# Optimization experiments

Measured on AMD Instinct MI355X. Metric: run time of the kernel, lower is better.

Reference implementation:

```python
import jax, jax.numpy as jnp
import numpy as np
import math

D_IN = 1024
D_OUT = 1024
NUM_HEADS = 16
D_HEAD = D_IN // NUM_HEADS


def setup_inputs() -> dict:
    key = jax.random.key(0)
    k1, k2, k3 = jax.random.split(key, 3)
    x = jax.random.normal(k1, (4, 2048, D_IN), dtype=jnp.float32)
    W_qkv = jax.random.normal(k2, (D_IN, 3 * D_OUT), dtype=jnp.float32) * (1.0 / math.sqrt(D_IN))
    b_qkv = jax.random.normal(k3, (3 * D_OUT,), dtype=jnp.float32) * 0.01
    return {"x": x, "W_qkv": W_qkv, "b_qkv": b_qkv}


def reference(x, W_qkv, b_qkv):
    B, S, _ = x.shape
    H, Dh = NUM_HEADS, D_HEAD
    # QKV projection: [B, S, 3*d_out]
    qkv = jnp.einsum('bsd,de->bse', x, W_qkv) + b_qkv
    # reshape per original: (B, S, H, 3*Dh) -> (B, H, S, 3*Dh)
    qkv = qkv.reshape(B, S, H, 3 * Dh).transpose(0, 2, 1, 3)
    q, k, v = jnp.split(qkv, 3, axis=-1)  # each [B, H, S, Dh]
    scale = 1.0 / math.sqrt(Dh)
    scores = jnp.einsum('bhqd,bhkd->bhqk', q, k) * scale
    attn = jax.nn.softmax(scores, axis=-1)
    ctx = jnp.einsum('bhqk,bhkd->bhqd', attn, v)  # [B, H, S, Dh]
    # (B, H, S, Dh) -> (B, S, H*Dh)
    return ctx.transpose(0, 2, 1, 3).reshape(B, S, D_OUT)
```

## Files before the change

### kernel.cpp

```cpp
#include <hip/hip_runtime.h>
#include <stdint.h>
#include <math.h>

#define D_IN   1024
#define NQKV   3072
#define NHEADS 16
#define DH     64
#define BATCH  4
#define SEQ    2048
#define MTOT   (BATCH*SEQ)

typedef __bf16    bf16x8 __attribute__((ext_vector_type(8)));
typedef _Float16  f16x8  __attribute__((ext_vector_type(8)));
typedef float     f32x4  __attribute__((ext_vector_type(4)));

typedef __attribute__((address_space(3))) unsigned short       lds_us;
typedef __attribute__((address_space(1))) const unsigned short glb_us;

__device__ __forceinline__ unsigned short f2bf(float f) {
    union { float f; uint32_t u; } c; c.f = f;
    uint32_t u = c.u;
    uint32_t r = u + 0x7fffu + ((u >> 16) & 1u);
    return (unsigned short)(r >> 16);
}
__device__ __forceinline__ float bf2f(unsigned short b) {
    union { uint32_t u; float f; } c; c.u = ((uint32_t)b) << 16;
    return c.f;
}
__device__ __forceinline__ uint32_t pkh(float a, float b) {
    auto h = __builtin_amdgcn_cvt_pkrtz(a, b);
    uint32_t u;
    __builtin_memcpy(&u, &h, 4);
    return u;
}

__global__ void k_convert_x(const float* __restrict__ x, unsigned short* __restrict__ xb) {
    int i = blockIdx.x * 256 + threadIdx.x;
    float4 v = ((const float4*)x)[i];
    ushort4 o;
    o.x = f2bf(v.x); o.y = f2bf(v.y); o.z = f2bf(v.z); o.w = f2bf(v.w);
    ((ushort4*)xb)[i] = o;
}

__global__ void k_convert_wt(const float* __restrict__ W, unsigned short* __restrict__ Wt) {
    __shared__ float tile[32][33];
    int tx = threadIdx.x, ty = threadIdx.y;
    int n0 = blockIdx.x * 32, k0 = blockIdx.y * 32;
    #pragma unroll
    for (int i = 0; i < 4; ++i) {
        int k = k0 + ty + i*8;
        tile[ty + i*8][tx] = W[(size_t)k * NQKV + n0 + tx];
    }
    __syncthreads();
    #pragma unroll
    for (int i = 0; i < 4; ++i) {
        int n = n0 + ty + i*8;
        Wt[(size_t)n * D_IN + k0 + tx] = f2bf(tile[tx][ty + i*8]);
    }
}

__global__ __launch_bounds__(256) void k_gemm_qkv(
    const unsigned short* __restrict__ A,
    const unsigned short* __restrict__ Bt,
    const float* __restrict__ bias,
    unsigned short* __restrict__ C)
{
    __shared__ __align__(16) unsigned short As[128*32];
    __shared__ __align__(16) unsigned short Bs[128*32];
    const int t = threadIdx.x;
    const int wave = t >> 6, lane = t & 63, quad = lane >> 4, l15 = lane & 15;
    const int wm = wave >> 1, wn = wave & 1;
    const int m0 = blockIdx.y * 128, n0 = blockIdx.x * 128;
    const int crow = lane >> 2;
    const int ccol = (lane & 3) << 3;

    f32x4 acc[4][4] = {};
    lds_us* As3 = (lds_us*)As;
    lds_us* Bs3 = (lds_us*)Bs;

    for (int k0 = 0; k0 < D_IN; k0 += 32) {
        #pragma unroll
        for (int j = 0; j < 2; ++j) {
            int chunk = wave*2 + j;
            const unsigned short* ga = A  + (size_t)(m0 + chunk*16 + crow)*D_IN + k0 + ccol;
            const unsigned short* gb = Bt + (size_t)(n0 + chunk*16 + crow)*D_IN + k0 + ccol;
            __builtin_amdgcn_global_load_lds((glb_us*)ga, As3 + chunk*512, 16, 0, 0);
            __builtin_amdgcn_global_load_lds((glb_us*)gb, Bs3 + chunk*512, 16, 0, 0);
        }
        __syncthreads();
        bf16x8 a[4], b[4];
        #pragma unroll
        for (int tm = 0; tm < 4; ++tm)
            a[tm] = *(const bf16x8*)(&As[(wm*64 + tm*16 + l15)*32 + quad*8]);
        #pragma unroll
        for (int tn = 0; tn < 4; ++tn)
            b[tn] = *(const bf16x8*)(&Bs[(wn*64 + tn*16 + l15)*32 + quad*8]);
        #pragma unroll
        for (int tm = 0; tm < 4; ++tm)
            #pragma unroll
            for (int tn = 0; tn < 4; ++tn)
                acc[tm][tn] = __builtin_amdgcn_mfma_f32_16x16x32_bf16(a[tm], b[tn], acc[tm][tn], 0, 0, 0);
        __syncthreads();
    }
    const float qs = 0.125f * 1.44269504089f;
    #pragma unroll
    for (int tn = 0; tn < 4; ++tn) {
        int col = n0 + wn*64 + tn*16 + l15;
        float bv = bias[col];
        float s = ((col % 192) < 64) ? qs : 1.0f;
        #pragma unroll
        for (int tm = 0; tm < 4; ++tm) {
            #pragma unroll
            for (int r = 0; r < 4; ++r) {
                int row = m0 + wm*64 + tm*16 + quad*4 + r;
                C[(size_t)row*NQKV + col] = f2bf((acc[tm][tn][r] + bv) * s);
            }
        }
    }
}

#define TP 66
__global__ __launch_bounds__(256) void k_transpose_v(
    const unsigned short* __restrict__ qkv,
    unsigned short* __restrict__ vtg)
{
    __shared__ unsigned short T[64*TP];
    const int t = threadIdx.x;
    const int bh = blockIdx.y, b = bh >> 4, h = bh & 15;
    const int s0 = blockIdx.x * 64;
    const unsigned short* src = qkv + (size_t)(b*SEQ + s0)*NQKV + h*(3*DH) + 2*DH;
    #pragma unroll
    for (int i = 0; i < 2; ++i) {
        int idx = t + i*256;
        int s = idx >> 3, c = (idx & 7) << 3;
        uint4 v = *(const uint4*)(src + (size_t)s*NQKV + c);
        unsigned short* dst = &T[s*TP + c];
        const unsigned short* pv = (const unsigned short*)&v;
        #pragma unroll
        for (int j = 0; j < 8; ++j) {
            _Float16 hv = (_Float16)bf2f(pv[j]);
            dst[j] = *(unsigned short*)&hv;
        }
    }
    __syncthreads();
    unsigned short* out = vtg + (size_t)bh * DH * SEQ + s0;
    #pragma unroll
    for (int i = 0; i < 16; ++i) {
        int idx = t + i*256;
        int d = idx >> 6, s = idx & 63;
        out[(size_t)d * SEQ + s] = T[s*TP + d];
    }
}

#define PPAD 40
#define OPAD 72
__global__ __launch_bounds__(256, 2) void k_attn(
    const unsigned short* __restrict__ qkv,
    const unsigned short* __restrict__ vtg,
    float* __restrict__ out)
{
    __shared__ __align__(16) unsigned short PO[4*64*OPAD];
    __shared__ float Lp[4*64];

    const int t = threadIdx.x;
    const int wave = t >> 6, lane = t & 63, quad = lane >> 4, l15 = lane & 15;
    const int bh = blockIdx.y, b = bh >> 4, h = bh & 15;
    const int m0 = blockIdx.x * 64;
    const unsigned short* base  = qkv + (size_t)(b*SEQ)*NQKV + h*(3*DH);
    const unsigned short* kbase = base + DH;
    const unsigned short* vbase = vtg + (size_t)bh * DH * SEQ;

    bf16x8 qb[4][2];
    #pragma unroll
    for (int tq = 0; tq < 4; ++tq) {
        const unsigned short* qrow = base + (size_t)(m0 + tq*16 + l15) * NQKV;
        qb[tq][0] = *(const bf16x8*)(qrow + quad*8);
        qb[tq][1] = *(const bf16x8*)(qrow + 32 + quad*8);
    }

    f32x4 o[4][4] = {};
    float lp[4] = {0.f, 0.f, 0.f, 0.f};
    unsigned short* pw = &PO[wave*64*PPAD];

    bf16x8 kf[2][2][2];
    f16x8  vf[2][4];
    {
        int key0 = wave*32;
        #pragma unroll
        for (int tk = 0; tk < 2; ++tk) {
            const unsigned short* kr = kbase + (size_t)(key0 + tk*16 + l15)*NQKV;
            kf[0][tk][0] = *(const bf16x8*)(kr + quad*8);
            kf[0][tk][1] = *(const bf16x8*)(kr + 32 + quad*8);
        }
        #pragma unroll
        for (int td = 0; td < 4; ++td)
            vf[0][td] = *(const f16x8*)(vbase + (size_t)(td*16 + l15)*SEQ + key0 + quad*8);
    }

    #pragma unroll 2
    for (int it = 0; it < 16; ++it) {
        const int cur = it & 1, nxt = cur ^ 1;
        if (it < 15) {
            int key0 = (it+1)*128 + wave*32;
            #pragma unroll
            for (int tk = 0; tk < 2; ++tk) {
                const unsigned short* kr = kbase + (size_t)(key0 + tk*16 + l15)*NQKV;
                kf[nxt][tk][0] = *(const bf16x8*)(kr + quad*8);
                kf[nxt][tk][1] = *(const bf16x8*)(kr + 32 + quad*8);
            }
            #pragma unroll
            for (int td = 0; td < 4; ++td)
                vf[nxt][td] = *(const f16x8*)(vbase + (size_t)(td*16 + l15)*SEQ + key0 + quad*8);
        }
        #pragma unroll
        for (int tk = 0; tk < 2; ++tk) {
            #pragma unroll
            for (int tq = 0; tq < 4; ++tq) {
                f32x4 a = {};
                a = __builtin_amdgcn_mfma_f32_16x16x32_bf16(kf[cur][tk][0], qb[tq][0], a, 0, 0, 0);
                a = __builtin_amdgcn_mfma_f32_16x16x32_bf16(kf[cur][tk][1], qb[tq][1], a, 0, 0, 0);
                float p0 = exp2f(a[0]), p1 = exp2f(a[1]);
                float p2 = exp2f(a[2]), p3 = exp2f(a[3]);
                lp[tq] += (p0 + p1) + (p2 + p3);
                uint2 u; u.x = pkh(p0, p1); u.y = pkh(p2, p3);
                *(uint2*)(&pw[(tq*16 + l15)*PPAD + tk*16 + quad*4]) = u;
            }
        }
        f16x8 pb[4];
        #pragma unroll
        for (int tq = 0; tq < 4; ++tq)
            pb[tq] = *(const f16x8*)(&pw[(tq*16 + l15)*PPAD + quad*8]);
        #pragma unroll
        for (int td = 0; td < 4; ++td)
            #pragma unroll
            for (int tq = 0; tq < 4; ++tq)
                o[td][tq] = __builtin_amdgcn_mfma_f32_16x16x32_f16(vf[cur][td], pb[tq], o[td][tq], 0, 0, 0);
    }

    #pragma unroll
    for (int tq = 0; tq < 4; ++tq) {
        float s = lp[tq];
        s += __shfl_xor(s, 16);
        s += __shfl_xor(s, 32);
        if (quad == 0) Lp[wave*64 + tq*16 + l15] = s;
    }
    __syncthreads();
    {
        unsigned short* ow = &PO[wave*64*OPAD];
        #pragma unroll
        for (int td = 0; td < 4; ++td)
            #pragma unroll
            for (int tq = 0; tq < 4; ++tq) {
                uint2 u; u.x = pkh(o[td][tq][0], o[td][tq][1]); u.y = pkh(o[td][tq][2], o[td][tq][3]);
                *(uint2*)(&ow[(tq*16 + l15)*OPAD + td*16 + quad*4]) = u;
            }
    }
    __syncthreads();
    float* outb = out + (size_t)(b*SEQ + m0) * (NHEADS*DH) + h*DH;
    #pragma unroll
    for (int i = 0; i < 16; ++i) {
        int idx = t + i*256;
        int q = idx >> 6, d = idx & 63;
        float lt = Lp[q] + Lp[64 + q] + Lp[128 + q] + Lp[192 + q];
        float s = 0.f;
        #pragma unroll
        for (int w2 = 0; w2 < 4; ++w2) {
            _Float16 hv = *(const _Float16*)&PO[(w2*64 + q)*OPAD + d];
            s += (float)hv;
        }
        outb[(size_t)q * (NHEADS*DH) + d] = s / lt;
    }
}

extern "C" void kernel_launch(void* const* d_in, const int* in_sizes, int n_in,
                              void* d_out, int out_size, void* d_ws, size_t ws_size,
                              hipStream_t stream) {
    const float* x    = (const float*)d_in[0];
    const float* W    = (const float*)d_in[1];
    const float* bias = (const float*)d_in[2];
    float* out = (float*)d_out;

    unsigned short* xb  = (unsigned short*)d_ws;
    unsigned short* Wt  = xb  + (size_t)MTOT * D_IN;
    unsigned short* qkv = Wt  + (size_t)NQKV * D_IN;
    unsigned short* vtg = xb;

    hipLaunchKernelGGL(k_convert_x,   dim3(MTOT*D_IN/4/256), dim3(256),    0, stream, x, xb);
    hipLaunchKernelGGL(k_convert_wt,  dim3(NQKV/32, D_IN/32), dim3(32, 8), 0, stream, W, Wt);
    hipLaunchKernelGGL(k_gemm_qkv,    dim3(NQKV/128, MTOT/128), dim3(256), 0, stream, xb, Wt, bias, qkv);
    hipLaunchKernelGGL(k_transpose_v, dim3(SEQ/64, BATCH*NHEADS), dim3(256), 0, stream, qkv, vtg);
    hipLaunchKernelGGL(k_attn,        dim3(SEQ/64, BATCH*NHEADS), dim3(256), 0, stream, qkv, vtg, out);
}
```

Before: 299.3 us.

## Single-buffer K/V fragments with staggered prefetch, raise occupancy, add MFMA priority

The attention loop drops its double-buffered K/V register fragments. Each K tile is now reloaded right after its QK MFMAs, and V is reloaded after the PV MFMAs, which cuts register pressure so launch bounds can request 3 blocks per CU. MFMA sections are wrapped in s_setprio so matrix work is favoured across waves. The grid is also transposed so blocks that share a head are spread across the first dimension, which changes L2 locality. The cost is less latency hiding per wave, since loads now land only one phase ahead, and more reliance on occupancy to cover it.

```diff
diff --git a/kernel.cpp b/kernel.cpp
--- a/kernel.cpp
+++ b/kernel.cpp
@@ -126,8 +126,8 @@
 {
     __shared__ unsigned short T[64*TP];
     const int t = threadIdx.x;
-    const int bh = blockIdx.y, b = bh >> 4, h = bh & 15;
-    const int s0 = blockIdx.x * 64;
+    const int bh = blockIdx.x, b = bh >> 4, h = bh & 15;
+    const int s0 = blockIdx.y * 64;
     const unsigned short* src = qkv + (size_t)(b*SEQ + s0)*NQKV + h*(3*DH) + 2*DH;
     #pragma unroll
     for (int i = 0; i < 2; ++i) {
@@ -154,7 +154,7 @@
 
 #define PPAD 40
 #define OPAD 72
-__global__ __launch_bounds__(256, 2) void k_attn(
+__global__ __launch_bounds__(256, 3) void k_attn(
     const unsigned short* __restrict__ qkv,
     const unsigned short* __restrict__ vtg,
     float* __restrict__ out)
@@ -164,8 +164,8 @@
 
     const int t = threadIdx.x;
     const int wave = t >> 6, lane = t & 63, quad = lane >> 4, l15 = lane & 15;
-    const int bh = blockIdx.y, b = bh >> 4, h = bh & 15;
-    const int m0 = blockIdx.x * 64;
+    const int bh = blockIdx.x, b = bh >> 4, h = bh & 15;
+    const int m0 = blockIdx.y * 64;
     const unsigned short* base  = qkv + (size_t)(b*SEQ)*NQKV + h*(3*DH);
     const unsigned short* kbase = base + DH;
     const unsigned short* vbase = vtg + (size_t)bh * DH * SEQ;
@@ -182,59 +182,59 @@
     float lp[4] = {0.f, 0.f, 0.f, 0.f};
     unsigned short* pw = &PO[wave*64*PPAD];
 
-    bf16x8 kf[2][2][2];
-    f16x8  vf[2][4];
+    bf16x8 kf[2][2];
+    f16x8  vf[4];
     {
         int key0 = wave*32;
         #pragma unroll
         for (int tk = 0; tk < 2; ++tk) {
             const unsigned short* kr = kbase + (size_t)(key0 + tk*16 + l15)*NQKV;
-            kf[0][tk][0] = *(const bf16x8*)(kr + quad*8);
-            kf[0][tk][1] = *(const bf16x8*)(kr + 32 + quad*8);
+            kf[tk][0] = *(const bf16x8*)(kr + quad*8);
+            kf[tk][1] = *(const bf16x8*)(kr + 32 + quad*8);
         }
         #pragma unroll
         for (int td = 0; td < 4; ++td)
-            vf[0][td] = *(const f16x8*)(vbase + (size_t)(td*16 + l15)*SEQ + key0 + quad*8);
-    }
-
-    #pragma unroll 2
+            vf[td] = *(const f16x8*)(vbase + (size_t)(td*16 + l15)*SEQ + key0 + quad*8);
+    }
+
     for (int it = 0; it < 16; ++it) {
-        const int cur = it & 1, nxt = cur ^ 1;
-        if (it < 15) {
-            int key0 = (it+1)*128 + wave*32;
-            #pragma unroll
-            for (int tk = 0; tk < 2; ++tk) {
-                const unsigned short* kr = kbase + (size_t)(key0 + tk*16 + l15)*NQKV;
-                kf[nxt][tk][0] = *(const bf16x8*)(kr + quad*8);
-                kf[nxt][tk][1] = *(const bf16x8*)(kr + 32 + quad*8);
-            }
-            #pragma unroll
-            for (int td = 0; td < 4; ++td)
-                vf[nxt][td] = *(const f16x8*)(vbase + (size_t)(td*16 + l15)*SEQ + key0 + quad*8);
-        }
         #pragma unroll
         for (int tk = 0; tk < 2; ++tk) {
             #pragma unroll
             for (int tq = 0; tq < 4; ++tq) {
                 f32x4 a = {};
-                a = __builtin_amdgcn_mfma_f32_16x16x32_bf16(kf[cur][tk][0], qb[tq][0], a, 0, 0, 0);
-                a = __builtin_amdgcn_mfma_f32_16x16x32_bf16(kf[cur][tk][1], qb[tq][1], a, 0, 0, 0);
+                __builtin_amdgcn_s_setprio(1);
+                a = __builtin_amdgcn_mfma_f32_16x16x32_bf16(kf[tk][0], qb[tq][0], a, 0, 0, 0);
+                a = __builtin_amdgcn_mfma_f32_16x16x32_bf16(kf[tk][1], qb[tq][1], a, 0, 0, 0);
+                __builtin_amdgcn_s_setprio(0);
                 float p0 = exp2f(a[0]), p1 = exp2f(a[1]);
                 float p2 = exp2f(a[2]), p3 = exp2f(a[3]);
                 lp[tq] += (p0 + p1) + (p2 + p3);
                 uint2 u; u.x = pkh(p0, p1); u.y = pkh(p2, p3);
                 *(uint2*)(&pw[(tq*16 + l15)*PPAD + tk*16 + quad*4]) = u;
             }
-        }
-        f16x8 pb[4];
-        #pragma unroll
-        for (int tq = 0; tq < 4; ++tq)
-            pb[tq] = *(const f16x8*)(&pw[(tq*16 + l15)*PPAD + quad*8]);
-        #pragma unroll
-        for (int td = 0; td < 4; ++td)
-            #pragma unroll
-            for (int tq = 0; tq < 4; ++tq)
-                o[td][tq] = __builtin_amdgcn_mfma_f32_16x16x32_f16(vf[cur][td], pb[tq], o[td][tq], 0, 0, 0);
+            if (it < 15) {
+                int key0 = (it+1)*128 + wave*32;
+                const unsigned short* kr = kbase + (size_t)(key0 + tk*16 + l15)*NQKV;
+                kf[tk][0] = *(const bf16x8*)(kr + quad*8);
+                kf[tk][1] = *(const bf16x8*)(kr + 32 + quad*8);
+            }
+        }
+        #pragma unroll
+        for (int tq = 0; tq < 4; ++tq) {
+            f16x8 pb = *(const f16x8*)(&pw[(tq*16 + l15)*PPAD + quad*8]);
+            __builtin_amdgcn_s_setprio(1);
+            #pragma unroll
+            for (int td = 0; td < 4; ++td)
+                o[td][tq] = __builtin_amdgcn_mfma_f32_16x16x32_f16(vf[td], pb, o[td][tq], 0, 0, 0);
+            __builtin_amdgcn_s_setprio(0);
+        }
+        if (it < 15) {
+            int key0 = (it+1)*128 + wave*32;
+            #pragma unroll
+            for (int td = 0; td < 4; ++td)
+                vf[td] = *(const f16x8*)(vbase + (size_t)(td*16 + l15)*SEQ + key0 + quad*8);
+        }
     }
 
     #pragma unroll
@@ -288,6 +288,6 @@
     hipLaunchKernelGGL(k_convert_x,   dim3(MTOT*D_IN/4/256), dim3(256),    0, stream, x, xb);
     hipLaunchKernelGGL(k_convert_wt,  dim3(NQKV/32, D_IN/32), dim3(32, 8), 0, stream, W, Wt);
     hipLaunchKernelGGL(k_gemm_qkv,    dim3(NQKV/128, MTOT/128), dim3(256), 0, stream, xb, Wt, bias, qkv);
-    hipLaunchKernelGGL(k_transpose_v, dim3(SEQ/64, BATCH*NHEADS), dim3(256), 0, stream, qkv, vtg);
-    hipLaunchKernelGGL(k_attn,        dim3(SEQ/64, BATCH*NHEADS), dim3(256), 0, stream, qkv, vtg, out);
-}
+    hipLaunchKernelGGL(k_transpose_v, dim3(BATCH*NHEADS, SEQ/64), dim3(256), 0, stream, qkv, vtg);
+    hipLaunchKernelGGL(k_attn,        dim3(BATCH*NHEADS, SEQ/64), dim3(256), 0, stream, qkv, vtg, out);
+}
```

Result: slower. 331.8 us (+10.9%).
